# Kernel tuning notes

Hardware: AMD Instinct MI355X
Metric: run time of the kernel (lower is better)

## Reference

```python
import jax, jax.numpy as jnp
import numpy as np

N_NODES = 500000
EMB = 32
K = 10          # sampled neighbors per node (num_sample in source)
BATCH = 100000


def setup_inputs() -> dict:
    key = jax.random.key(0)
    k1, k2, k3, k4, k5 = jax.random.split(key, 5)
    # xavier-ish scale for weights [emb, 2*emb]
    w_scale = jnp.sqrt(2.0 / (EMB + 2 * EMB)).astype(jnp.float32)
    emb = jax.random.normal(k1, (N_NODES, EMB), dtype=jnp.float32)
    W1 = jax.random.normal(k2, (EMB, 2 * EMB), dtype=jnp.float32) * w_scale
    W2 = jax.random.normal(k3, (EMB, 2 * EMB), dtype=jnp.float32) * w_scale
    node_batch = jax.random.randint(k4, (BATCH,), 0, N_NODES)
    neigh = jax.random.randint(k5, (N_NODES, K), 0, N_NODES)
    return {"emb": emb, "W1": W1, "W2": W2,
            "node_batch": node_batch, "neigh": neigh}


def _sage_layer(self_feat, agg_feat, W):
    # SageLayer.forward: relu(W.mm(cat([self, agg], 1).t()).t()) == relu(cat @ W.T)
    combined = jnp.concatenate([self_feat, agg_feat], axis=1)  # [n, 2E]
    return jax.nn.relu(combined @ W.T)                          # [n, E]


def reference(emb, W1, W2, node_batch, neigh):
    # Layer 1: MEAN aggregation of K sampled neighbors for every node
    # (mask.mm(embed_matrix) with row-normalized 0/1 mask == gather + mean)
    agg1 = jnp.take(emb, neigh, axis=0).mean(axis=1)   # [N, E]
    h1 = _sage_layer(emb, agg1, W1)                    # [N, E]
    # Layer 2: aggregate over neighbors of the batch nodes using layer-1 embeds
    nb_neigh = jnp.take(neigh, node_batch, axis=0)     # [B, K]
    agg2 = jnp.take(h1, nb_neigh, axis=0).mean(axis=1) # [B, E]
    out = _sage_layer(jnp.take(h1, node_batch, axis=0), agg2, W2)  # [B, E]
    return out
```

## Files before the change

kernel.cpp:

```cpp
#include <hip/hip_runtime.h>

#define EMBD 32
#define KN 10

template<bool REMAP>
__global__ __launch_bounds__(256, 2)
void sage_layer(const float* __restrict__ feat,
                const float* __restrict__ W,
                const int*   __restrict__ neigh,
                const int*   __restrict__ remap,
                float*       __restrict__ out,
                int n_rows)
{
    __shared__ float sh[64][257];
    const int tid  = threadIdx.x;
    const int wid  = tid >> 6;
    const int lane = tid & 63;
    const int half = lane >> 5;
    const int j    = lane & 31;
    const int row0 = blockIdx.x << 8;

    #pragma unroll 4
    for (int i = 0; i < 32; ++i) {
        int t = (wid << 6) + (i << 1) + half;
        int r = row0 + t;
        if (r >= n_rows) r = n_rows - 1;
        const int node = REMAP ? remap[r] : r;
        const float self = feat[node * EMBD + j];
        const int* nb = neigh + node * KN;
        float agg = 0.f;
        #pragma unroll
        for (int k = 0; k < KN; ++k) {
            int idx = nb[k];
            agg += feat[idx * EMBD + j];
        }
        sh[j][t]      = self;
        sh[32 + j][t] = agg * 0.1f;
    }
    __syncthreads();

    float comb[64];
    #pragma unroll
    for (int jj = 0; jj < 64; ++jj)
        comb[jj] = sh[jj][tid];

    const int  r     = row0 + tid;
    const bool valid = (r < n_rows);
    float* orow = out + (size_t)r * EMBD;

    for (int e4 = 0; e4 < 8; ++e4) {
        float oq[4];
        #pragma unroll
        for (int q = 0; q < 4; ++q) {
            const float* wr = W + (e4 * 4 + q) * 64;
            float acc = 0.f;
            #pragma unroll
            for (int jj = 0; jj < 64; ++jj)
                acc = fmaf(comb[jj], wr[jj], acc);
            oq[q] = acc > 0.f ? acc : 0.f;
        }
        if (valid)
            *(float4*)(orow + e4 * 4) = make_float4(oq[0], oq[1], oq[2], oq[3]);
    }
}

extern "C" void kernel_launch(void* const* d_in, const int* in_sizes, int n_in,
                              void* d_out, int out_size, void* d_ws, size_t ws_size,
                              hipStream_t stream)
{
    const float* emb        = (const float*)d_in[0];
    const float* W1         = (const float*)d_in[1];
    const float* W2         = (const float*)d_in[2];
    const int*   node_batch = (const int*)  d_in[3];
    const int*   neigh      = (const int*)  d_in[4];

    const int N = in_sizes[0] / EMBD;
    const int B = in_sizes[3];

    float* h1 = (float*)d_ws;

    sage_layer<false><<<(N + 255) / 256, 256, 0, stream>>>(
        emb, W1, neigh, nullptr, h1, N);

    sage_layer<true><<<(B + 255) / 256, 256, 0, stream>>>(
        h1, W2, neigh, node_batch, (float*)d_out, B);
}
```

Baseline: 270.6 us.

## Store embeddings and layer-1 output in bf16 and retile the SAGE layer to 64-row blocks

A new kernel converts the fp32 embedding table to bf16 in workspace, and both layers then gather bf16 rows, halving the bytes moved by the random neighbor gathers. Layer 1 writes h1 as bf16. Each block now covers 64 rows with 4 waves, each wave computing 8 output columns, which shrinks shared memory and the per-thread register array so occupancy can rise. The cost is an extra pass that reads and writes the full table, plus reduced precision of features and intermediates, which may exceed the tolerance.

```diff
diff --git a/kernel.cpp b/kernel.cpp
--- a/kernel.cpp
+++ b/kernel.cpp
@@ -3,64 +3,93 @@
 #define EMBD 32
 #define KN 10
 
-template<bool REMAP>
-__global__ __launch_bounds__(256, 2)
-void sage_layer(const float* __restrict__ feat,
+__device__ __forceinline__ float bf2f(unsigned short u) {
+    union { unsigned int u; float f; } c; c.u = ((unsigned int)u) << 16; return c.f;
+}
+__device__ __forceinline__ unsigned short f2bf(float f) {
+    union { float f; unsigned int u; } c; c.f = f;
+    unsigned int u = c.u + 0x7FFFu + ((c.u >> 16) & 1u);
+    return (unsigned short)(u >> 16);
+}
+
+__global__ __launch_bounds__(256)
+void cvt_bf16_kernel(const float4* __restrict__ in, ushort4* __restrict__ out, int n4)
+{
+    int i = blockIdx.x * 256 + threadIdx.x;
+    if (i < n4) {
+        float4 v = in[i];
+        ushort4 o;
+        o.x = f2bf(v.x); o.y = f2bf(v.y); o.z = f2bf(v.z); o.w = f2bf(v.w);
+        out[i] = o;
+    }
+}
+
+template<bool REMAP, bool OUT_BF16>
+__global__ __launch_bounds__(256, 4)
+void sage_layer(const unsigned short* __restrict__ feat,
                 const float* __restrict__ W,
                 const int*   __restrict__ neigh,
                 const int*   __restrict__ remap,
-                float*       __restrict__ out,
+                void*        __restrict__ out,
                 int n_rows)
 {
-    __shared__ float sh[64][257];
+    __shared__ float sh[64][65];
     const int tid  = threadIdx.x;
-    const int wid  = tid >> 6;
-    const int lane = tid & 63;
-    const int half = lane >> 5;
-    const int j    = lane & 31;
-    const int row0 = blockIdx.x << 8;
+    const int row0 = blockIdx.x << 6;
 
-    #pragma unroll 4
-    for (int i = 0; i < 32; ++i) {
-        int t = (wid << 6) + (i << 1) + half;
-        int r = row0 + t;
-        if (r >= n_rows) r = n_rows - 1;
-        const int node = REMAP ? remap[r] : r;
-        const float self = feat[node * EMBD + j];
-        const int* nb = neigh + node * KN;
-        float agg = 0.f;
-        #pragma unroll
-        for (int k = 0; k < KN; ++k) {
-            int idx = nb[k];
-            agg += feat[idx * EMBD + j];
+    {
+        const int hw = tid >> 5;
+        const int j  = tid & 31;
+        #pragma unroll 2
+        for (int i = 0; i < 8; ++i) {
+            const int rl = hw * 8 + i;
+            int r = row0 + rl;
+            if (r >= n_rows) r = n_rows - 1;
+            const int node = REMAP ? remap[r] : r;
+            const float self = bf2f(feat[node * EMBD + j]);
+            const int* nb = neigh + node * KN;
+            float agg = 0.f;
+            #pragma unroll
+            for (int k = 0; k < KN; ++k)
+                agg += bf2f(feat[nb[k] * EMBD + j]);
+            sh[j][rl]      = self;
+            sh[32 + j][rl] = agg * 0.1f;
         }
-        sh[j][t]      = self;
-        sh[32 + j][t] = agg * 0.1f;
     }
     __syncthreads();
 
-    float comb[64];
-    #pragma unroll
-    for (int jj = 0; jj < 64; ++jj)
-        comb[jj] = sh[jj][tid];
+    const int row = tid & 63;
+    const int wid = __builtin_amdgcn_readfirstlane(tid >> 6);
+    const float* Wb = W + wid * 8 * 64;
 
-    const int  r     = row0 + tid;
-    const bool valid = (r < n_rows);
-    float* orow = out + (size_t)r * EMBD;
+    float acc[8] = {0.f,0.f,0.f,0.f,0.f,0.f,0.f,0.f};
+    #pragma unroll 8
+    for (int jj = 0; jj < 64; ++jj) {
+        const float c = sh[jj][row];
+        #pragma unroll
+        for (int q = 0; q < 8; ++q)
+            acc[q] = fmaf(c, Wb[q * 64 + jj], acc[q]);
+    }
 
-    for (int e4 = 0; e4 < 8; ++e4) {
-        float oq[4];
-        #pragma unroll
-        for (int q = 0; q < 4; ++q) {
-            const float* wr = W + (e4 * 4 + q) * 64;
-            float acc = 0.f;
+    const int r = row0 + row;
+    if (r < n_rows) {
+        if (OUT_BF16) {
+            unsigned int pk[4];
             #pragma unroll
-            for (int jj = 0; jj < 64; ++jj)
-                acc = fmaf(comb[jj], wr[jj], acc);
-            oq[q] = acc > 0.f ? acc : 0.f;
+            for (int q = 0; q < 4; ++q) {
+                float a0 = fmaxf(acc[2*q],     0.f);
+                float a1 = fmaxf(acc[2*q + 1], 0.f);
+                pk[q] = (unsigned int)f2bf(a0) | ((unsigned int)f2bf(a1) << 16);
+            }
+            uint4* dst = (uint4*)((unsigned short*)out + (size_t)r * EMBD + wid * 8);
+            *dst = make_uint4(pk[0], pk[1], pk[2], pk[3]);
+        } else {
+            float* dst = (float*)out + (size_t)r * EMBD + wid * 8;
+            ((float4*)dst)[0] = make_float4(fmaxf(acc[0],0.f), fmaxf(acc[1],0.f),
+                                            fmaxf(acc[2],0.f), fmaxf(acc[3],0.f));
+            ((float4*)dst)[1] = make_float4(fmaxf(acc[4],0.f), fmaxf(acc[5],0.f),
+                                            fmaxf(acc[6],0.f), fmaxf(acc[7],0.f));
         }
-        if (valid)
-            *(float4*)(orow + e4 * 4) = make_float4(oq[0], oq[1], oq[2], oq[3]);
     }
 }
 
@@ -77,11 +106,16 @@
     const int N = in_sizes[0] / EMBD;
     const int B = in_sizes[3];
 
-    float* h1 = (float*)d_ws;
+    unsigned short* emb_bf = (unsigned short*)d_ws;
+    unsigned short* h1_bf  = emb_bf + (size_t)N * EMBD;
 
-    sage_layer<false><<<(N + 255) / 256, 256, 0, stream>>>(
-        emb, W1, neigh, nullptr, h1, N);
+    const int n4 = (N * EMBD) / 4;
+    cvt_bf16_kernel<<<(n4 + 255) / 256, 256, 0, stream>>>(
+        (const float4*)emb, (ushort4*)emb_bf, n4);
 
-    sage_layer<true><<<(B + 255) / 256, 256, 0, stream>>>(
-        h1, W2, neigh, node_batch, (float*)d_out, B);
+    sage_layer<false, true><<<(N + 63) / 64, 256, 0, stream>>>(
+        emb_bf, W1, neigh, nullptr, (void*)h1_bf, N);
+
+    sage_layer<true, false><<<(B + 63) / 64, 256, 0, stream>>>(
+        h1_bf, W2, neigh, node_batch, d_out, B);
 }
```

After: 236.5 us. -12.6%, faster.
